# Kernel optimization log

Hardware: AMD Instinct MI355X
Metric: run time of the kernel (lower is better)

## Reference

```python
import jax, jax.numpy as jnp
import numpy as np

# model constants (from source: PRE/COMM/OUT sizes; chosen: G, D, E, T, NF)
G, D, E, T = 128, 64, 8, 4096          # group feats, per-elevator feats, n elevators, timesteps
PRE, CI, CH, OUT, NF = 256, 128, 128, 128, 64
ROUNDS, DROPOFF = 3, 0.333
IN = G + D                              # elevator_input_size = 192
OIN = 2 * CH + IN                       # out-LSTM input = 448


def _cell(x, h, c, Wih, Whh, b):
    # torch nn.LSTM cell, gate order i,f,g,o; b = b_ih + b_hh
    g = x @ Wih.T + h @ Whh.T + b
    i, f, gg, o = jnp.split(g, 4, axis=-1)
    c2 = jax.nn.sigmoid(f) * c + jax.nn.sigmoid(i) * jnp.tanh(gg)
    h2 = jax.nn.sigmoid(o) * jnp.tanh(c2)
    return h2, c2


def _forward(features, pre_h0, pre_c0, out_h0, out_c0,
             Wih_p0, Whh_p0, b_p0, Wih_p1, Whh_p1, b_p1, Wfc, bfc,
             Wih_c0, Whh_c0, b_c0, Wih_c1, Whh_c1, b_c1,
             Wih_o, Whh_o, b_o, Wtar, btar, Wdir, bdir):
    def step(carry, feat):
        pre_h, pre_c, out_h, out_c = carry
        group = feat[:G]
        ele = feat[G:].reshape(E, D)
        x = jnp.concatenate([jnp.broadcast_to(group, (E, G)), ele], axis=-1)  # [E, IN]
        # preprocess: 2-layer LSTM single step, batched over elevators
        h0, c0 = _cell(x, pre_h[:, 0], pre_c[:, 0], Wih_p0, Whh_p0, b_p0)
        h1, c1 = _cell(h0, pre_h[:, 1], pre_c[:, 1], Wih_p1, Whh_p1, b_p1)
        pre_out = jax.nn.leaky_relu(h1 @ Wfc.T + bfc, 0.05)                   # [E, CI]
        new_pre_h = jnp.stack([h0, h1], axis=1)
        new_pre_c = jnp.stack([c0, c1], axis=1)
        # alpha-decayed communication rounds: sequential scan over elevators
        ch = jnp.zeros((2, CH), jnp.float32)
        cc = jnp.zeros((2, CH), jnp.float32)
        alpha = 1.0
        for _ in range(ROUNDS):
            def comm_step(cs, xin, alpha=alpha):
                ch_, cc_ = cs
                h0n, c0n = _cell(xin, ch_[0], cc_[0], Wih_c0, Whh_c0, b_c0)
                h0b = (1.0 - alpha) * ch_[0] + alpha * h0n
                c0b = (1.0 - alpha) * cc_[0] + alpha * c0n
                h1n, c1n = _cell(h0b, ch_[1], cc_[1], Wih_c1, Whh_c1, b_c1)
                h1b = (1.0 - alpha) * ch_[1] + alpha * h1n
                c1b = (1.0 - alpha) * cc_[1] + alpha * c1n
                return (jnp.stack([h0b, h1b]), jnp.stack([c0b, c1b])), None
            (ch, cc), _ = jax.lax.scan(comm_step, (ch, cc), pre_out)
            alpha *= DROPOFF
        group_dec = cc.reshape(-1)                                            # [2*CH] = comm_c.flatten()
        out_in = jnp.concatenate([jnp.broadcast_to(group_dec, (E, 2 * CH)), x], axis=-1)  # [E, OIN]
        oh, oc = _cell(out_in, out_h, out_c, Wih_o, Whh_o, b_o)
        tar = jax.nn.softmax(oh @ Wtar.T + btar, axis=-1)                     # [E, NF]
        dr = jax.nn.softmax(oh @ Wdir.T + bdir, axis=-1)                      # [E, 3]
        return (new_pre_h, new_pre_c, oh, oc), (tar, dr)

    _, (tar_seq, dir_seq) = jax.lax.scan(step, (pre_h0, pre_c0, out_h0, out_c0), features)
    return tar_seq, dir_seq


def setup_inputs() -> dict:
    key = jax.random.key(0)
    ks = iter(jax.random.split(key, 32))
    p = lambda *s: jax.random.normal(next(ks), s, jnp.float32) * 0.05
    return {
        "features": jax.random.normal(next(ks), (T, G + E * D), jnp.float32),
        "pre_h0": jnp.zeros((E, 2, PRE), jnp.float32),
        "pre_c0": jnp.zeros((E, 2, PRE), jnp.float32),
        "out_h0": jnp.zeros((E, OUT), jnp.float32),
        "out_c0": jnp.zeros((E, OUT), jnp.float32),
        "Wih_p0": p(4 * PRE, IN), "Whh_p0": p(4 * PRE, PRE), "b_p0": p(4 * PRE),
        "Wih_p1": p(4 * PRE, PRE), "Whh_p1": p(4 * PRE, PRE), "b_p1": p(4 * PRE),
        "Wfc": p(CI, PRE), "bfc": p(CI),
        "Wih_c0": p(4 * CH, CI), "Whh_c0": p(4 * CH, CH), "b_c0": p(4 * CH),
        "Wih_c1": p(4 * CH, CH), "Whh_c1": p(4 * CH, CH), "b_c1": p(4 * CH),
        "Wih_o": p(4 * OUT, OIN), "Whh_o": p(4 * OUT, OUT), "b_o": p(4 * OUT),
        "Wtar": p(NF, OUT), "btar": p(NF),
        "Wdir": p(3, OUT), "bdir": p(3),
    }


def reference(features, pre_h0, pre_c0, out_h0, out_c0,
              Wih_p0, Whh_p0, b_p0, Wih_p1, Whh_p1, b_p1, Wfc, bfc,
              Wih_c0, Whh_c0, b_c0, Wih_c1, Whh_c1, b_c1,
              Wih_o, Whh_o, b_o, Wtar, btar, Wdir, bdir):
    return _forward(features, pre_h0, pre_c0, out_h0, out_c0,
                    Wih_p0, Whh_p0, b_p0, Wih_p1, Whh_p1, b_p1, Wfc, bfc,
                    Wih_c0, Whh_c0, b_c0, Wih_c1, Whh_c1, b_c1,
                    Wih_o, Whh_o, b_o, Wtar, btar, Wdir, bdir)
```

## Files before the change

### kernel.cpp

```cpp
#include <hip/hip_runtime.h>
#include <hip/hip_bf16.h>

#define T_   4096
#define E_   8
#define NCON 56

typedef unsigned long long ull;

__device__ __forceinline__ float sigm(float x)  { return 1.0f / (1.0f + __expf(-x)); }
__device__ __forceinline__ float tanh_(float x) { return 1.0f - 2.0f / (__expf(2.0f * x) + 1.0f); }

__device__ __forceinline__ ull aload64(const ull* p) {
  return __hip_atomic_load(p, __ATOMIC_RELAXED, __HIP_MEMORY_SCOPE_AGENT);
}
__device__ __forceinline__ int aload32(const int* p) {
  return __hip_atomic_load(p, __ATOMIC_RELAXED, __HIP_MEMORY_SCOPE_AGENT);
}
__device__ __forceinline__ float aloadf(const float* p) {
  return __hip_atomic_load(p, __ATOMIC_RELAXED, __HIP_MEMORY_SCOPE_AGENT);
}
__device__ __forceinline__ float tagf(float h, unsigned g) {
  return __uint_as_float((__float_as_uint(h) & ~7u) | g);
}
__device__ __forceinline__ bool tagok4(const ull* v, unsigned g) {
  bool ok = true;
  #pragma unroll
  for (int i = 0; i < 4; ++i) {
    unsigned lo = (unsigned)v[i], hi = (unsigned)(v[i] >> 32);
    ok &= ((lo & 7u) == g) & ((hi & 7u) == g);
  }
  return ok;
}
__device__ __forceinline__ void lbar() {
  asm volatile("s_waitcnt lgkmcnt(0)\n\ts_barrier" ::: "memory");
}

#define FMA_8(ACC, W, VA, VB)                                   \
  ACC[0] = fmaf((W), (VA).x, ACC[0]); ACC[1] = fmaf((W), (VA).y, ACC[1]); \
  ACC[2] = fmaf((W), (VA).z, ACC[2]); ACC[3] = fmaf((W), (VA).w, ACC[3]); \
  ACC[4] = fmaf((W), (VB).x, ACC[4]); ACC[5] = fmaf((W), (VB).y, ACC[5]); \
  ACC[6] = fmaf((W), (VB).z, ACC[6]); ACC[7] = fmaf((W), (VB).w, ACC[7]);

__global__ void initK(const float* __restrict__ Wih_p0, const float* __restrict__ Whh_p0,
                      const float* __restrict__ Wih_p1, const float* __restrict__ Whh_p1,
                      const float* __restrict__ Wih_c0, const float* __restrict__ Whh_c0,
                      const float* __restrict__ Wih_c1, const float* __restrict__ Whh_c1,
                      const float* __restrict__ Wih_o,
                      float* wt_p0, float* wt_p1, float* wt_c0, float* wt_c1,
                      float* wt_o1, float* wt_o2, int* zbase) {
  const int NW = 458752 + 524288 + 131072 + 131072 + 131072 + 98304;
  const int NZ = 65536 + 65536 + 16384 + 65536 + 16384;
  const int NTOT = NW + NZ;
  const int gsz = gridDim.x * blockDim.x;
  for (int i = blockIdx.x * blockDim.x + threadIdx.x; i < NTOT; i += gsz) {
    int idx = i;
    if (idx < 458752) { int k = idx >> 10, c = idx & 1023;
      int wg = c >> 5, r5 = c & 31, gate = r5 >> 3, jl = r5 & 7;
      int col = gate * 256 + wg * 8 + jl;
      wt_p0[idx] = (k < 192) ? Wih_p0[col * 192 + k] : Whh_p0[col * 256 + (k - 192)]; continue; }
    idx -= 458752;
    if (idx < 524288) { int k = idx >> 10, c = idx & 1023;
      int wg = c >> 5, r5 = c & 31, gate = r5 >> 3, jl = r5 & 7;
      int col = gate * 256 + wg * 8 + jl;
      wt_p1[idx] = (k < 256) ? Wih_p1[col * 256 + k] : Whh_p1[col * 256 + (k - 256)]; continue; }
    idx -= 524288;
    if (idx < 131072) { int k = idx >> 9, r = idx & 511;
      wt_c0[idx] = (k < 128) ? Wih_c0[r * 128 + k] : Whh_c0[r * 128 + (k - 128)]; continue; }
    idx -= 131072;
    if (idx < 131072) { int k = idx >> 9, r = idx & 511;
      wt_c1[idx] = (k < 128) ? Wih_c1[r * 128 + k] : Whh_c1[r * 128 + (k - 128)]; continue; }
    idx -= 131072;
    if (idx < 131072) { int k = idx >> 9, r = idx & 511;
      wt_o1[idx] = Wih_o[r * 448 + k]; continue; }
    idx -= 131072;
    if (idx < 98304) { int k = idx >> 9, r = idx & 511;
      wt_o2[idx] = Wih_o[r * 448 + 256 + k]; continue; }
    idx -= 98304;
    zbase[idx] = 0;
  }
}

__global__ void opre2K(const float* __restrict__ feat, const float* __restrict__ wt_o2,
                       __hip_bfloat16* __restrict__ opre2) {
  __shared__ float xb[192 * 8];
  const int t = blockIdx.x, tid = threadIdx.x;
  const float* ft = feat + (size_t)t * 640;
  for (int idx = tid; idx < 192 * 8; idx += 256) {
    int k = idx >> 3, e = idx & 7;
    xb[idx] = (k < 128) ? ft[k] : ft[128 + e * 64 + (k - 128)];
  }
  __syncthreads();
  const int r = tid;
  float A0[8] = {0,0,0,0,0,0,0,0};
  float A1[8] = {0,0,0,0,0,0,0,0};
  const float4* x4 = (const float4*)xb;
  #pragma unroll 2
  for (int k = 0; k < 192; ++k) {
    float w0 = wt_o2[k * 512 + r];
    float w1 = wt_o2[k * 512 + 256 + r];
    float4 a = x4[k * 2], b = x4[k * 2 + 1];
    FMA_8(A0, w0, a, b);
    FMA_8(A1, w1, a, b);
  }
  #pragma unroll
  for (int e = 0; e < 8; ++e) {
    opre2[((size_t)t * 8 + e) * 512 + r]       = __float2bfloat16(A0[e]);
    opre2[((size_t)t * 8 + e) * 512 + 256 + r] = __float2bfloat16(A1[e]);
  }
}

__device__ __forceinline__ void comm_cell(
    const float* __restrict__ wt, const float* __restrict__ bias,
    const float* xin, float* hL, float* cL, float* glb, float* hout,
    float alpha, int tid) {
  const int r = tid;
  float A0[8] = {0,0,0,0,0,0,0,0};
  float A1[8] = {0,0,0,0,0,0,0,0};
  const float4* x4 = (const float4*)xin;
  #pragma unroll 2
  for (int k = 0; k < 128; ++k) {
    float w0 = wt[k * 512 + r];
    float w1 = wt[k * 512 + 256 + r];
    float4 a = x4[k * 2], b = x4[k * 2 + 1];
    FMA_8(A0, w0, a, b);
    FMA_8(A1, w1, a, b);
  }
  const float4* h4 = (const float4*)hL;
  #pragma unroll 2
  for (int k = 0; k < 128; ++k) {
    float w0 = wt[(128 + k) * 512 + r];
    float w1 = wt[(128 + k) * 512 + 256 + r];
    float4 a = h4[k * 2], b = h4[k * 2 + 1];
    FMA_8(A0, w0, a, b);
    FMA_8(A1, w1, a, b);
  }
  {
    float4* g4 = (float4*)glb;
    g4[r * 2]             = make_float4(A0[0], A0[1], A0[2], A0[3]);
    g4[r * 2 + 1]         = make_float4(A0[4], A0[5], A0[6], A0[7]);
    g4[(256 + r) * 2]     = make_float4(A1[0], A1[1], A1[2], A1[3]);
    g4[(256 + r) * 2 + 1] = make_float4(A1[4], A1[5], A1[6], A1[7]);
  }
  __syncthreads();
  for (int idx = tid; idx < 1024; idx += 256) {
    int jj = idx >> 3, tt = idx & 7;
    float gi = glb[jj * 8 + tt]         + bias[jj];
    float gf = glb[(128 + jj) * 8 + tt] + bias[128 + jj];
    float gg = glb[(256 + jj) * 8 + tt] + bias[256 + jj];
    float go = glb[(384 + jj) * 8 + tt] + bias[384 + jj];
    float cold = cL[idx], hold = hL[idx];
    float c2 = sigm(gf) * cold + sigm(gi) * tanh_(gg);
    float h2 = sigm(go) * tanh_(c2);
    float hb = fmaf(alpha, h2 - hold, hold);
    float cb = fmaf(alpha, c2 - cold, cold);
    hL[idx] = hb; cL[idx] = cb;
    if (hout) hout[idx] = hb;
  }
  __syncthreads();
}

__launch_bounds__(256, 1)
__global__ void megaK(const float* __restrict__ feat,
                      const float* __restrict__ pre_h0, const float* __restrict__ pre_c0,
                      const float* __restrict__ wt_p0, const float* __restrict__ wt_p1,
                      const float* __restrict__ b_p0, const float* __restrict__ b_p1,
                      float* __restrict__ h0ringL, float* __restrict__ h0ringG,
                      float* __restrict__ h1ringL,
                      float* __restrict__ h1all, int* __restrict__ flagsBC,
                      const float* __restrict__ Wfc, const float* __restrict__ bfc,
                      const float* __restrict__ wt_c0, const float* __restrict__ wt_c1,
                      const float* __restrict__ b_c0, const float* __restrict__ b_c1,
                      const float* __restrict__ wt_o1, const float* __restrict__ b_o,
                      float* __restrict__ opre1, int* __restrict__ flagC,
                      const __hip_bfloat16* __restrict__ opre2,
                      const float* __restrict__ Whh_o, const float* __restrict__ out_h0,
                      const float* __restrict__ out_c0, float* __restrict__ oh_g) {
  __shared__ float lds[38912];
  const int role = blockIdx.x & 7, idx = blockIdx.x >> 3;
  const int tid = threadIdx.x;

  if (role == 0) {
    const int wg = idx;
    float* wl  = lds;
    float* xb0 = lds + 14336;
    float* xb1 = lds + 15872;
    float* hsf = lds + 17408;
    float* gl  = lds + 19456;
    const int r5 = tid & 31, kq = tid >> 5;
    for (int i2 = tid; i2 < 14336; i2 += 256)
      wl[i2] = wt_p0[(size_t)(i2 >> 5) * 1024 + wg * 32 + (i2 & 31)];
    float creg = 0.f, bi = 0.f, bff = 0.f, bg = 0.f, bo = 0.f;
    if (tid < 64) {
      const int jl = tid >> 3, e = tid & 7, j = wg * 8 + jl;
      creg = pre_c0[(e * 2 + 0) * 256 + j];
      bi = b_p0[j]; bff = b_p0[256 + j]; bg = b_p0[512 + j]; bo = b_p0[768 + j];
    }
    for (int i2 = tid; i2 < 2048; i2 += 256) {
      int k = i2 >> 3, e = i2 & 7;
      hsf[i2] = pre_h0[(e * 2 + 0) * 256 + k];
    }
    for (int i2 = tid; i2 < 1536; i2 += 256) {
      int k = i2 >> 3, e = i2 & 7;
      xb0[i2] = (k < 128) ? feat[k] : feat[128 + e * 64 + (k - 128)];
    }
    __syncthreads();
    const bool own = ((tid >> 3) == wg);
    float Ax[8] = {0,0,0,0,0,0,0,0};
    {
      const float4* x4 = (const float4*)xb0;
      #pragma unroll
      for (int k = kq * 24; k < kq * 24 + 24; ++k) {
        float w = wl[k * 32 + r5];
        float4 a = x4[k * 2], b = x4[k * 2 + 1];
        FMA_8(Ax, w, a, b);
      }
    }
    for (int t = 0; t < T_; ++t) {
      float px[6];
      if (t + 1 < T_) {
        const float* ft1 = feat + (size_t)(t + 1) * 640;
        #pragma unroll
        for (int i = 0; i < 6; ++i) {
          int i2 = tid + i * 256; int k = i2 >> 3, e = i2 & 7;
          px[i] = (k < 128) ? ft1[k] : ft1[128 + e * 64 + (k - 128)];
        }
      }
      float A[8];
      #pragma unroll
      for (int i = 0; i < 8; ++i) A[i] = Ax[i];
      {
        const float4* h4 = (const float4*)hsf;
        #pragma unroll
        for (int k2 = 0; k2 < 32; ++k2) {
          const int k = kq * 32 + k2;
          float w = wl[(192 + k) * 32 + r5];
          float4 a = h4[k * 2], b = h4[k * 2 + 1];
          FMA_8(A, w, a, b);
        }
      }
      {
        float4* g4 = (float4*)gl;
        g4[(kq * 32 + r5) * 2]     = make_float4(A[0], A[1], A[2], A[3]);
        g4[(kq * 32 + r5) * 2 + 1] = make_float4(A[4], A[5], A[6], A[7]);
      }
      if (t + 1 < T_) {
        float* xbN = ((t + 1) & 1) ? xb1 : xb0;
        #pragma unroll
        for (int i = 0; i < 6; ++i) xbN[tid + i * 256] = px[i];
      }
      if (t >= 24 && tid >= 224) {
        const int t2 = (t - 24) | 7;
        const int* fp = flagsBC + ((size_t)(t2 & 63) * 32 + (tid - 224)) * 32;
        while (aload32(fp) < t2 + 1) __builtin_amdgcn_s_sleep(16);
      }
      lbar();
      const unsigned g = ((unsigned)(t >> 5) % 7u) + 1u;
      float* ringS = h0ringL + (size_t)(t & 31) * 2048;
      if (tid < 64) {
        float s0 = 0.f, s1 = 0.f, s2 = 0.f, s3 = 0.f;
        #pragma unroll
        for (int q = 0; q < 8; ++q) {
          s0 += gl[q * 256 + tid];       s1 += gl[q * 256 + 64 + tid];
          s2 += gl[q * 256 + 128 + tid]; s3 += gl[q * 256 + 192 + tid];
        }
        float c2 = sigm(s1 + bff) * creg + sigm(s0 + bi) * tanh_(s2 + bg);
        float h2 = sigm(s3 + bo) * tanh_(c2);
        creg = c2;
        float tv = tagf(h2, g);
        __hip_atomic_store(&ringS[wg * 64 + tid], tv,
                           __ATOMIC_RELAXED, __HIP_MEMORY_SCOPE_AGENT);
        __hip_atomic_store(&h0ringG[(size_t)(t & 31) * 2048 + wg * 64 + tid], tv,
                           __ATOMIC_RELAXED, __HIP_MEMORY_SCOPE_AGENT);
        hsf[wg * 64 + tid] = h2;
      }
      if (t + 1 >= T_) break;
      ull v[4];
      const ull* rp = (const ull*)ringS + tid * 4;
      if (!own) {
        #pragma unroll
        for (int i = 0; i < 4; ++i) v[i] = aload64(rp + i);
      }
      #pragma unroll
      for (int i = 0; i < 8; ++i) Ax[i] = 0.f;
      {
        const float4* x4 = (const float4*)(((t + 1) & 1) ? xb1 : xb0);
        #pragma unroll
        for (int k = kq * 24; k < kq * 24 + 24; ++k) {
          float w = wl[k * 32 + r5];
          float4 a = x4[k * 2], b = x4[k * 2 + 1];
          FMA_8(Ax, w, a, b);
        }
      }
      if (!own) {
        while (!tagok4(v, g)) {
          __builtin_amdgcn_s_sleep(1);
          #pragma unroll
          for (int i = 0; i < 4; ++i) v[i] = aload64(rp + i);
        }
        ull* d8 = (ull*)hsf;
        #pragma unroll
        for (int i = 0; i < 4; ++i) d8[tid * 4 + i] = v[i];
      }
      lbar();
    }
  } else if (role == 1) {
    const int wgl = idx;
    float* wl  = lds;
    float* xh0 = lds + 16384;
    float* hsf = lds + 18432;
    float* gl  = lds + 20480;
    const int r5 = tid & 31, kq = tid >> 5;
    for (int i2 = tid; i2 < 16384; i2 += 256)
      wl[i2] = wt_p1[(size_t)(i2 >> 5) * 1024 + wgl * 32 + (i2 & 31)];
    float creg = 0.f, bi = 0.f, bff = 0.f, bg = 0.f, bo = 0.f;
    if (tid < 64) {
      const int jl = tid >> 3, e = tid & 7, j = wgl * 8 + jl;
      creg = pre_c0[(e * 2 + 1) * 256 + j];
      bi = b_p1[j]; bff = b_p1[256 + j]; bg = b_p1[512 + j]; bo = b_p1[768 + j];
    }
    for (int i2 = tid; i2 < 2048; i2 += 256) {
      int k = i2 >> 3, e = i2 & 7;
      hsf[i2] = pre_h0[(e * 2 + 1) * 256 + k];
    }
    __syncthreads();
    const bool own = ((tid >> 3) == wgl);
    ull pv[4];
    {
      ull v[4];
      const ull* rp = (const ull*)h0ringG + tid * 4;
      #pragma unroll
      for (int i = 0; i < 4; ++i) v[i] = aload64(rp + i);
      while (!tagok4(v, 1u)) {
        __builtin_amdgcn_s_sleep(1);
        #pragma unroll
        for (int i = 0; i < 4; ++i) v[i] = aload64(rp + i);
      }
      ull* d8 = (ull*)xh0;
      #pragma unroll
      for (int i = 0; i < 4; ++i) d8[tid * 4 + i] = v[i];
    }
    lbar();
    float Ax[8] = {0,0,0,0,0,0,0,0};
    {
      const float4* x4 = (const float4*)xh0;
      #pragma unroll
      for (int k = kq * 32; k < kq * 32 + 32; ++k) {
        float w = wl[k * 32 + r5];
        float4 a = x4[k * 2], b = x4[k * 2 + 1];
        FMA_8(Ax, w, a, b);
      }
    }
    {
      const ull* rp = (const ull*)(h0ringG + 2048) + tid * 4;
      #pragma unroll
      for (int i = 0; i < 4; ++i) pv[i] = aload64(rp + i);
      while (!tagok4(pv, 1u)) {
        __builtin_amdgcn_s_sleep(1);
        #pragma unroll
        for (int i = 0; i < 4; ++i) pv[i] = aload64(rp + i);
      }
    }
    lbar();
    for (int t = 0; t < T_; ++t) {
      float A[8];
      #pragma unroll
      for (int i = 0; i < 8; ++i) A[i] = Ax[i];
      {
        const float4* h4 = (const float4*)hsf;
        #pragma unroll
        for (int k2 = 0; k2 < 32; ++k2) {
          const int k = kq * 32 + k2;
          float w = wl[(256 + k) * 32 + r5];
          float4 a = h4[k * 2], b = h4[k * 2 + 1];
          FMA_8(A, w, a, b);
        }
      }
      {
        float4* g4 = (float4*)gl;
        g4[(kq * 32 + r5) * 2]     = make_float4(A[0], A[1], A[2], A[3]);
        g4[(kq * 32 + r5) * 2 + 1] = make_float4(A[4], A[5], A[6], A[7]);
      }
      if (t + 1 < T_) {
        ull* d8 = (ull*)xh0;
        #pragma unroll
        for (int i = 0; i < 4; ++i) d8[tid * 4 + i] = pv[i];
      }
      lbar();
      const unsigned g1 = ((unsigned)(t >> 3) % 7u) + 1u;
      float* ringS = h1ringL + (size_t)(t & 7) * 2048;
      if (tid < 64) {
        float s0 = 0.f, s1 = 0.f, s2 = 0.f, s3 = 0.f;
        #pragma unroll
        for (int q = 0; q < 8; ++q) {
          s0 += gl[q * 256 + tid];       s1 += gl[q * 256 + 64 + tid];
          s2 += gl[q * 256 + 128 + tid]; s3 += gl[q * 256 + 192 + tid];
        }
        float c2 = sigm(s1 + bff) * creg + sigm(s0 + bi) * tanh_(s2 + bg);
        float h2 = sigm(s3 + bo) * tanh_(c2);
        creg = c2;
        __hip_atomic_store(&ringS[wgl * 64 + tid], tagf(h2, g1),
                           __ATOMIC_RELAXED, __HIP_MEMORY_SCOPE_AGENT);
        hsf[wgl * 64 + tid] = h2;
        __hip_atomic_store(&h1all[(size_t)t * 2048 + wgl * 64 + tid], h2,
                           __ATOMIC_RELAXED, __HIP_MEMORY_SCOPE_AGENT);
        if ((t & 7) == 7) {
          asm volatile("s_waitcnt vmcnt(0)" ::: "memory");
          if (tid == 0)
            __hip_atomic_store(&flagsBC[((size_t)(t & 63) * 32 + wgl) * 32], t + 1,
                               __ATOMIC_RELAXED, __HIP_MEMORY_SCOPE_AGENT);
        }
      }
      if (t + 1 >= T_) break;
      ull w1[4];
      const ull* rp1 = (const ull*)ringS + tid * 4;
      if (!own) {
        #pragma unroll
        for (int i = 0; i < 4; ++i) w1[i] = aload64(rp1 + i);
      }
      #pragma unroll
      for (int i = 0; i < 8; ++i) Ax[i] = 0.f;
      {
        const float4* x4 = (const float4*)xh0;
        #pragma unroll
        for (int k = kq * 32; k < kq * 32 + 32; ++k) {
          float w = wl[k * 32 + r5];
          float4 a = x4[k * 2], b = x4[k * 2 + 1];
          FMA_8(Ax, w, a, b);
        }
      }
      if (!own) {
        while (!tagok4(w1, g1)) {
          __builtin_amdgcn_s_sleep(1);
          #pragma unroll
          for (int i = 0; i < 4; ++i) w1[i] = aload64(rp1 + i);
        }
        ull* d8 = (ull*)hsf;
        #pragma unroll
        for (int i = 0; i < 4; ++i) d8[tid * 4 + i] = w1[i];
      }
      if (t + 2 < T_) {
        const unsigned g0 = ((unsigned)((t + 2) >> 5) % 7u) + 1u;
        const ull* rp0 = (const ull*)(h0ringG + (size_t)((t + 2) & 31) * 2048) + tid * 4;
        #pragma unroll
        for (int i = 0; i < 4; ++i) pv[i] = aload64(rp0 + i);
        while (!tagok4(pv, g0)) {
          __builtin_amdgcn_s_sleep(1);
          #pragma unroll
          for (int i = 0; i < 4; ++i) pv[i] = aload64(rp0 + i);
        }
      }
      lbar();
    }
  } else if (role == 2 && idx < 8) {
    const int e = idx;
    float* wlds = lds;
    float* ohl  = lds + 32768;
    float* gl   = lds + 32896;
    for (int i2 = tid; i2 < 32768; i2 += 256) {
      int k = i2 >> 8, rr = i2 & 255;
      wlds[i2] = Whh_o[(256 + rr) * 128 + k];
    }
    float w[128];
    #pragma unroll
    for (int k = 0; k < 128; ++k) w[k] = Whh_o[tid * 128 + k];
    if (tid < 128) ohl[tid] = out_h0[e * 128 + tid];
    float creg = (tid < 128) ? out_c0[e * 128 + tid] : 0.f;
    __syncthreads();
    if (tid == 0) { while (aload32(&flagC[0]) == 0) __builtin_amdgcn_s_sleep(4); }
    __syncthreads();
    const int r0 = tid, r1 = tid + 256;
    float pa = aloadf(&opre1[r0]), pb = aloadf(&opre1[r1]);
    float qa = __bfloat162float(opre2[(size_t)e * 512 + r0]);
    float qb = __bfloat162float(opre2[(size_t)e * 512 + r1]);
    float na = aloadf(&opre1[512 + r0]), nb = aloadf(&opre1[512 + r1]);
    float ma = __bfloat162float(opre2[(size_t)(8 + e) * 512 + r0]);
    float mb = __bfloat162float(opre2[(size_t)(8 + e) * 512 + r1]);
    for (int t = 0; t < T_; ++t) {
      float a0 = pa + qa, a1 = pb + qb;
      pa = na; pb = nb; qa = ma; qb = mb;
      if ((t & 7) == 6 && t + 2 < T_) {
        if (tid == 0) { while (aload32(&flagC[((t + 2) >> 3) * 32]) == 0) __builtin_amdgcn_s_sleep(4); }
        __syncthreads();
      }
      if (t + 2 < T_) {
        na = aloadf(&opre1[(size_t)(t + 2) * 512 + r0]);
        nb = aloadf(&opre1[(size_t)(t + 2) * 512 + r1]);
        ma = __bfloat162float(opre2[((size_t)(t + 2) * 8 + e) * 512 + r0]);
        mb = __bfloat162float(opre2[((size_t)(t + 2) * 8 + e) * 512 + r1]);
      }
      const float4* o4 = (const float4*)ohl;
      #pragma unroll
      for (int kk = 0; kk < 32; ++kk) {
        float4 x = o4[kk];
        a0 = fmaf(w[kk * 4 + 0], x.x, a0); a0 = fmaf(w[kk * 4 + 1], x.y, a0);
        a0 = fmaf(w[kk * 4 + 2], x.z, a0); a0 = fmaf(w[kk * 4 + 3], x.w, a0);
        a1 = fmaf(wlds[(kk * 4 + 0) * 256 + tid], x.x, a1);
        a1 = fmaf(wlds[(kk * 4 + 1) * 256 + tid], x.y, a1);
        a1 = fmaf(wlds[(kk * 4 + 2) * 256 + tid], x.z, a1);
        a1 = fmaf(wlds[(kk * 4 + 3) * 256 + tid], x.w, a1);
      }
      gl[r0] = a0; gl[r1] = a1;
      __syncthreads();
      if (tid < 128) {
        float gi = gl[tid], gf = gl[128 + tid], gg = gl[256 + tid], go = gl[384 + tid];
        float c2 = sigm(gf) * creg + sigm(gi) * tanh_(gg);
        float h2 = sigm(go) * tanh_(c2);
        creg = c2;
        ohl[tid] = h2;
        oh_g[(size_t)t * 1024 + e * 128 + tid] = h2;
      }
      __syncthreads();
    }
  } else if (role >= 3) {
    const int cb = (role - 3) * 32 + idx;
    if (cb >= NCON) return;
    float* h1c    = lds;
    float* polAll = lds + 16384;
    float* ch0 = lds + 24576; float* cc0 = lds + 25600;
    float* ch1 = lds + 26624; float* cc1 = lds + 27648;
    float* h0b = lds + 28672;
    float* glb = lds + 29696;
    for (int chunk = cb; chunk < 512; chunk += NCON) {
      const int t0 = chunk * 8;
      if (tid < 32) {
        const int* fp = flagsBC + ((size_t)((t0 + 7) & 63) * 32 + tid) * 32;
        while (aload32(fp) < t0 + 8) __builtin_amdgcn_s_sleep(64);
      }
      __syncthreads();
      {
        const ull* src = (const ull*)(h1all + (size_t)t0 * 2048);
        ull* dst = (ull*)h1c;
        for (int i = tid; i < 8192; i += 256) dst[i] = aload64(src + i);
      }
      __syncthreads();
      {
        const int c = tid >> 1, half = tid & 1;
        const float bv = bfc[c];
        const float* wrow = Wfc + c * 256;
        for (int tt = 0; tt < 8; ++tt) {
          float a0 = bv, a1 = bv, a2 = bv, a3 = bv;
          const float4* h4 = (const float4*)(h1c + tt * 2048);
          #pragma unroll 4
          for (int k = 0; k < 256; ++k) {
            float wv = wrow[k];
            float4 x = h4[k * 2 + half];
            a0 = fmaf(wv, x.x, a0); a1 = fmaf(wv, x.y, a1);
            a2 = fmaf(wv, x.z, a2); a3 = fmaf(wv, x.w, a3);
          }
          float vv[4] = {a0, a1, a2, a3};
          #pragma unroll
          for (int i = 0; i < 4; ++i) {
            float v = vv[i];
            v = (v > 0.f) ? v : 0.05f * v;
            polAll[(half * 4 + i) * 1024 + c * 8 + tt] = v;
          }
        }
      }
      for (int i2 = tid; i2 < 1024; i2 += 256) { ch0[i2]=0.f; cc0[i2]=0.f; ch1[i2]=0.f; cc1[i2]=0.f; }
      __syncthreads();
      float alpha = 1.0f;
      for (int rd = 0; rd < 3; ++rd) {
        for (int e = 0; e < E_; ++e) {
          comm_cell(wt_c0, b_c0, polAll + e * 1024, ch0, cc0, glb, h0b, alpha, tid);
          comm_cell(wt_c1, b_c1, h0b, ch1, cc1, glb, nullptr, alpha, tid);
        }
        alpha *= 0.333f;
      }
      {
        const int r = tid;
        float A0[8], A1[8];
        #pragma unroll
        for (int tt = 0; tt < 8; ++tt) { A0[tt] = b_o[r]; A1[tt] = b_o[256 + r]; }
        const float4* c04 = (const float4*)cc0;
        const float4* c14 = (const float4*)cc1;
        #pragma unroll 2
        for (int k = 0; k < 128; ++k) {
          float w0 = wt_o1[k * 512 + r], w1 = wt_o1[k * 512 + 256 + r];
          float4 a = c04[k * 2], b = c04[k * 2 + 1];
          FMA_8(A0, w0, a, b);
          FMA_8(A1, w1, a, b);
        }
        #pragma unroll 2
        for (int k = 0; k < 128; ++k) {
          float w0 = wt_o1[(128 + k) * 512 + r], w1 = wt_o1[(128 + k) * 512 + 256 + r];
          float4 a = c14[k * 2], b = c14[k * 2 + 1];
          FMA_8(A0, w0, a, b);
          FMA_8(A1, w1, a, b);
        }
        #pragma unroll
        for (int tt = 0; tt < 8; ++tt) {
          __hip_atomic_store(&opre1[((size_t)(t0 + tt)) * 512 + r], A0[tt],
                             __ATOMIC_RELAXED, __HIP_MEMORY_SCOPE_AGENT);
          __hip_atomic_store(&opre1[((size_t)(t0 + tt)) * 512 + 256 + r], A1[tt],
                             __ATOMIC_RELAXED, __HIP_MEMORY_SCOPE_AGENT);
        }
      }
      __syncthreads();
      if (tid == 0)
        __hip_atomic_store(&flagC[chunk * 32], 1, __ATOMIC_RELAXED, __HIP_MEMORY_SCOPE_AGENT);
      __syncthreads();
    }
  }
}

__global__ void phaseD(const float* __restrict__ oh_g,
                       const float* __restrict__ Wtar, const float* __restrict__ btar,
                       const float* __restrict__ Wdir, const float* __restrict__ bdir,
                       float* __restrict__ outp) {
  __shared__ float ohl[1024];
  const int t = blockIdx.x, tid = threadIdx.x;
  for (int idx = tid; idx < 1024; idx += 64) ohl[idx] = oh_g[(size_t)t * 1024 + idx];
  __syncthreads();
  const int f = tid;
  for (int e = 0; e < E_; ++e) {
    float acc = btar[f];
    const float* wr = Wtar + f * 128;
    #pragma unroll 4
    for (int k = 0; k < 128; ++k) acc = fmaf(wr[k], ohl[e * 128 + k], acc);
    float m = acc;
    #pragma unroll
    for (int off = 32; off; off >>= 1) m = fmaxf(m, __shfl_xor(m, off, 64));
    float ex = __expf(acc - m);
    float s = ex;
    #pragma unroll
    for (int off = 32; off; off >>= 1) s += __shfl_xor(s, off, 64);
    outp[((size_t)t * 8 + e) * 64 + f] = ex / s;
  }
  if (tid < 8) {
    int e = tid;
    float d0 = bdir[0], d1 = bdir[1], d2 = bdir[2];
    #pragma unroll 4
    for (int k = 0; k < 128; ++k) {
      float x = ohl[e * 128 + k];
      d0 = fmaf(Wdir[k], x, d0);
      d1 = fmaf(Wdir[128 + k], x, d1);
      d2 = fmaf(Wdir[256 + k], x, d2);
    }
    float m = fmaxf(d0, fmaxf(d1, d2));
    float x0 = __expf(d0 - m), x1 = __expf(d1 - m), x2 = __expf(d2 - m);
    float s = x0 + x1 + x2;
    float* dp = outp + (size_t)T_ * 8 * 64 + ((size_t)t * 8 + e) * 3;
    dp[0] = x0 / s; dp[1] = x1 / s; dp[2] = x2 / s;
  }
}

extern "C" void kernel_launch(void* const* d_in, const int* in_sizes, int n_in,
                              void* d_out, int out_size, void* d_ws, size_t ws_size,
                              hipStream_t stream) {
  (void)in_sizes; (void)n_in; (void)out_size; (void)ws_size;
  const float* feat   = (const float*)d_in[0];
  const float* pre_h0 = (const float*)d_in[1];
  const float* pre_c0 = (const float*)d_in[2];
  const float* out_h0 = (const float*)d_in[3];
  const float* out_c0 = (const float*)d_in[4];
  const float* Wih_p0 = (const float*)d_in[5];
  const float* Whh_p0 = (const float*)d_in[6];
  const float* b_p0   = (const float*)d_in[7];
  const float* Wih_p1 = (const float*)d_in[8];
  const float* Whh_p1 = (const float*)d_in[9];
  const float* b_p1   = (const float*)d_in[10];
  const float* Wfc    = (const float*)d_in[11];
  const float* bfc    = (const float*)d_in[12];
  const float* Wih_c0 = (const float*)d_in[13];
  const float* Whh_c0 = (const float*)d_in[14];
  const float* b_c0   = (const float*)d_in[15];
  const float* Wih_c1 = (const float*)d_in[16];
  const float* Whh_c1 = (const float*)d_in[17];
  const float* b_c1   = (const float*)d_in[18];
  const float* Wih_o  = (const float*)d_in[19];
  const float* Whh_o  = (const float*)d_in[20];
  const float* b_o    = (const float*)d_in[21];
  const float* Wtar   = (const float*)d_in[22];
  const float* btar   = (const float*)d_in[23];
  const float* Wdir   = (const float*)d_in[24];
  const float* bdir   = (const float*)d_in[25];
  float* outp = (float*)d_out;

  float* ws = (float*)d_ws;
  size_t off = 0;
  float* opre1    = ws + off; off += (size_t)T_ * 512;
  float* oh_g     = ws + off; off += (size_t)T_ * E_ * 128;
  float* wt_p0    = ws + off; off += (size_t)448 * 1024;
  float* wt_p1    = ws + off; off += (size_t)512 * 1024;
  float* wt_c0    = ws + off; off += (size_t)256 * 512;
  float* wt_c1    = ws + off; off += (size_t)256 * 512;
  float* wt_o1    = ws + off; off += (size_t)256 * 512;
  float* wt_o2    = ws + off; off += (size_t)192 * 512;
  __hip_bfloat16* opre2 = (__hip_bfloat16*)(ws + off);
  off += (size_t)T_ * E_ * 512 / 2;
  float* h1all   = ws + off; off += (size_t)T_ * 2048;
  float* h0ringL = ws + off; off += (size_t)32 * 2048;
  float* h0ringG = ws + off; off += (size_t)32 * 2048;
  float* h1ringL = ws + off; off += (size_t)8 * 2048;
  int* flags    = (int*)(ws + off);
  int* flagsBC  = flags;
  int* flagC    = flags + (size_t)64 * 32 * 32;
  int* zbase    = (int*)h0ringL;

  initK<<<dim3(1024), dim3(256), 0, stream>>>(
      Wih_p0, Whh_p0, Wih_p1, Whh_p1, Wih_c0, Whh_c0, Wih_c1, Whh_c1, Wih_o,
      wt_p0, wt_p1, wt_c0, wt_c1, wt_o1, wt_o2, zbase);
  opre2K<<<dim3(T_), dim3(256), 0, stream>>>(feat, wt_o2, opre2);
  megaK<<<dim3(256), dim3(256), 0, stream>>>(
      feat, pre_h0, pre_c0, wt_p0, wt_p1, b_p0, b_p1,
      h0ringL, h0ringG, h1ringL, h1all, flagsBC,
      Wfc, bfc, wt_c0, wt_c1, b_c0, b_c1, wt_o1, b_o, opre1, flagC,
      opre2, Whh_o, out_h0, out_c0, oh_g);
  phaseD<<<dim3(T_), dim3(64), 0, stream>>>(oh_g, Wtar, btar, Wdir, bdir, outp);
}
```

Measured before the change: 15.56 ms.

## Remove per-step barrier in preprocess LSTM roles via double-buffered gate scratch

The two preprocess LSTM roles now double-buffer their gate-partial scratch (and, in layer 1, the input buffer), so the second workgroup barrier in each timestep can be dropped. Every thread now reads its full hidden-state slice back from the tagged ring, including the owning workgroup's own slice, instead of writing it locally, so no intra-block barrier is needed before the next step. The s_sleep back-off inside the spin-waits is removed to cut polling latency. In exchange, LDS use grows, global ring traffic rises slightly, and spinning becomes more aggressive, which can compete for memory bandwidth. Correctness now rests on the ring tags alone to order writes and reads across steps.

```diff
diff --git a/kernel.cpp b/kernel.cpp
--- a/kernel.cpp
+++ b/kernel.cpp
@@ -185,7 +185,8 @@
     float* xb0 = lds + 14336;
     float* xb1 = lds + 15872;
     float* hsf = lds + 17408;
-    float* gl  = lds + 19456;
+    float* gl0 = lds + 19456;
+    float* gl1 = lds + 21504;
     const int r5 = tid & 31, kq = tid >> 5;
     for (int i2 = tid; i2 < 14336; i2 += 256)
       wl[i2] = wt_p0[(size_t)(i2 >> 5) * 1024 + wg * 32 + (i2 & 31)];
@@ -204,7 +205,6 @@
       xb0[i2] = (k < 128) ? feat[k] : feat[128 + e * 64 + (k - 128)];
     }
     __syncthreads();
-    const bool own = ((tid >> 3) == wg);
     float Ax[8] = {0,0,0,0,0,0,0,0};
     {
       const float4* x4 = (const float4*)xb0;
@@ -238,8 +238,9 @@
           FMA_8(A, w, a, b);
         }
       }
-      {
-        float4* g4 = (float4*)gl;
+      float* glp = (t & 1) ? gl1 : gl0;
+      {
+        float4* g4 = (float4*)glp;
         g4[(kq * 32 + r5) * 2]     = make_float4(A[0], A[1], A[2], A[3]);
         g4[(kq * 32 + r5) * 2 + 1] = make_float4(A[4], A[5], A[6], A[7]);
       }
@@ -260,8 +261,8 @@
         float s0 = 0.f, s1 = 0.f, s2 = 0.f, s3 = 0.f;
         #pragma unroll
         for (int q = 0; q < 8; ++q) {
-          s0 += gl[q * 256 + tid];       s1 += gl[q * 256 + 64 + tid];
-          s2 += gl[q * 256 + 128 + tid]; s3 += gl[q * 256 + 192 + tid];
+          s0 += glp[q * 256 + tid];       s1 += glp[q * 256 + 64 + tid];
+          s2 += glp[q * 256 + 128 + tid]; s3 += glp[q * 256 + 192 + tid];
         }
         float c2 = sigm(s1 + bff) * creg + sigm(s0 + bi) * tanh_(s2 + bg);
         float h2 = sigm(s3 + bo) * tanh_(c2);
@@ -271,15 +272,12 @@
                            __ATOMIC_RELAXED, __HIP_MEMORY_SCOPE_AGENT);
         __hip_atomic_store(&h0ringG[(size_t)(t & 31) * 2048 + wg * 64 + tid], tv,
                            __ATOMIC_RELAXED, __HIP_MEMORY_SCOPE_AGENT);
-        hsf[wg * 64 + tid] = h2;
       }
       if (t + 1 >= T_) break;
       ull v[4];
       const ull* rp = (const ull*)ringS + tid * 4;
-      if (!own) {
-        #pragma unroll
-        for (int i = 0; i < 4; ++i) v[i] = aload64(rp + i);
-      }
+      #pragma unroll
+      for (int i = 0; i < 4; ++i) v[i] = aload64(rp + i);
       #pragma unroll
       for (int i = 0; i < 8; ++i) Ax[i] = 0.f;
       {
@@ -291,24 +289,24 @@
           FMA_8(Ax, w, a, b);
         }
       }
-      if (!own) {
-        while (!tagok4(v, g)) {
-          __builtin_amdgcn_s_sleep(1);
-          #pragma unroll
-          for (int i = 0; i < 4; ++i) v[i] = aload64(rp + i);
-        }
+      while (!tagok4(v, g)) {
+        #pragma unroll
+        for (int i = 0; i < 4; ++i) v[i] = aload64(rp + i);
+      }
+      {
         ull* d8 = (ull*)hsf;
         #pragma unroll
         for (int i = 0; i < 4; ++i) d8[tid * 4 + i] = v[i];
       }
-      lbar();
     }
   } else if (role == 1) {
     const int wgl = idx;
-    float* wl  = lds;
-    float* xh0 = lds + 16384;
-    float* hsf = lds + 18432;
-    float* gl  = lds + 20480;
+    float* wl   = lds;
+    float* xh0a = lds + 16384;
+    float* xh0b = lds + 18432;
+    float* hsf  = lds + 20480;
+    float* gl0  = lds + 22528;
+    float* gl1  = lds + 24576;
     const int r5 = tid & 31, kq = tid >> 5;
     for (int i2 = tid; i2 < 16384; i2 += 256)
       wl[i2] = wt_p1[(size_t)(i2 >> 5) * 1024 + wgl * 32 + (i2 & 31)];
@@ -323,7 +321,6 @@
       hsf[i2] = pre_h0[(e * 2 + 1) * 256 + k];
     }
     __syncthreads();
-    const bool own = ((tid >> 3) == wgl);
     ull pv[4];
     {
       ull v[4];
@@ -335,14 +332,14 @@
         #pragma unroll
         for (int i = 0; i < 4; ++i) v[i] = aload64(rp + i);
       }
-      ull* d8 = (ull*)xh0;
+      ull* d8 = (ull*)xh0a;
       #pragma unroll
       for (int i = 0; i < 4; ++i) d8[tid * 4 + i] = v[i];
     }
     lbar();
     float Ax[8] = {0,0,0,0,0,0,0,0};
     {
-      const float4* x4 = (const float4*)xh0;
+      const float4* x4 = (const float4*)xh0a;
       #pragma unroll
       for (int k = kq * 32; k < kq * 32 + 32; ++k) {
         float w = wl[k * 32 + r5];
@@ -360,7 +357,6 @@
         for (int i = 0; i < 4; ++i) pv[i] = aload64(rp + i);
       }
     }
-    lbar();
     for (int t = 0; t < T_; ++t) {
       float A[8];
       #pragma unroll
@@ -375,13 +371,14 @@
           FMA_8(A, w, a, b);
         }
       }
-      {
-        float4* g4 = (float4*)gl;
+      float* glp = (t & 1) ? gl1 : gl0;
+      {
+        float4* g4 = (float4*)glp;
         g4[(kq * 32 + r5) * 2]     = make_float4(A[0], A[1], A[2], A[3]);
         g4[(kq * 32 + r5) * 2 + 1] = make_float4(A[4], A[5], A[6], A[7]);
       }
       if (t + 1 < T_) {
-        ull* d8 = (ull*)xh0;
+        ull* d8 = (ull*)(((t + 1) & 1) ? xh0b : xh0a);
         #pragma unroll
         for (int i = 0; i < 4; ++i) d8[tid * 4 + i] = pv[i];
       }
@@ -392,15 +389,14 @@
         float s0 = 0.f, s1 = 0.f, s2 = 0.f, s3 = 0.f;
         #pragma unroll
         for (int q = 0; q < 8; ++q) {
-          s0 += gl[q * 256 + tid];       s1 += gl[q * 256 + 64 + tid];
-          s2 += gl[q * 256 + 128 + tid]; s3 += gl[q * 256 + 192 + tid];
+          s0 += glp[q * 256 + tid];       s1 += glp[q * 256 + 64 + tid];
+          s2 += glp[q * 256 + 128 + tid]; s3 += glp[q * 256 + 192 + tid];
         }
         float c2 = sigm(s1 + bff) * creg + sigm(s0 + bi) * tanh_(s2 + bg);
         float h2 = sigm(s3 + bo) * tanh_(c2);
         creg = c2;
         __hip_atomic_store(&ringS[wgl * 64 + tid], tagf(h2, g1),
                            __ATOMIC_RELAXED, __HIP_MEMORY_SCOPE_AGENT);
-        hsf[wgl * 64 + tid] = h2;
         __hip_atomic_store(&h1all[(size_t)t * 2048 + wgl * 64 + tid], h2,
                            __ATOMIC_RELAXED, __HIP_MEMORY_SCOPE_AGENT);
         if ((t & 7) == 7) {
@@ -413,14 +409,12 @@
       if (t + 1 >= T_) break;
       ull w1[4];
       const ull* rp1 = (const ull*)ringS + tid * 4;
-      if (!own) {
-        #pragma unroll
-        for (int i = 0; i < 4; ++i) w1[i] = aload64(rp1 + i);
-      }
+      #pragma unroll
+      for (int i = 0; i < 4; ++i) w1[i] = aload64(rp1 + i);
       #pragma unroll
       for (int i = 0; i < 8; ++i) Ax[i] = 0.f;
       {
-        const float4* x4 = (const float4*)xh0;
+        const float4* x4 = (const float4*)(((t + 1) & 1) ? xh0b : xh0a);
         #pragma unroll
         for (int k = kq * 32; k < kq * 32 + 32; ++k) {
           float w = wl[k * 32 + r5];
@@ -428,12 +422,11 @@
           FMA_8(Ax, w, a, b);
         }
       }
-      if (!own) {
-        while (!tagok4(w1, g1)) {
-          __builtin_amdgcn_s_sleep(1);
-          #pragma unroll
-          for (int i = 0; i < 4; ++i) w1[i] = aload64(rp1 + i);
-        }
+      while (!tagok4(w1, g1)) {
+        #pragma unroll
+        for (int i = 0; i < 4; ++i) w1[i] = aload64(rp1 + i);
+      }
+      {
         ull* d8 = (ull*)hsf;
         #pragma unroll
         for (int i = 0; i < 4; ++i) d8[tid * 4 + i] = w1[i];
@@ -444,12 +437,10 @@
         #pragma unroll
         for (int i = 0; i < 4; ++i) pv[i] = aload64(rp0 + i);
         while (!tagok4(pv, g0)) {
-          __builtin_amdgcn_s_sleep(1);
           #pragma unroll
           for (int i = 0; i < 4; ++i) pv[i] = aload64(rp0 + i);
         }
       }
-      lbar();
     }
   } else if (role == 2 && idx < 8) {
     const int e = idx;
```

New measurement: 15.57 ms. About the same (+0.1%).
